# Kernel tuning notes

Hardware: AMD Instinct MI355X
Metric: run time of the kernel (lower is better)

The kernel has to match this reference:

```python
import jax, jax.numpy as jnp
import numpy as np

N_NODES = 50000
N_EDGES = 800000
F_IN = 128
HEADS = 2
C_HID = 64
N_GRAPHS = 32
NEG_SLOPE = 0.2
LP_LAYERS = 2
LP_ALPHA = 0.5


def gatv2_conv(x, src, dst, W_l, W_r, att, bias):
    """GATv2Conv (concat=True), edge_attr=None, self-loops already in src/dst."""
    H, C = att.shape
    N = x.shape[0]
    xl = (x @ W_l).reshape(N, H, C)  # source-side transform (x_j)
    xr = (x @ W_r).reshape(N, H, C)  # target-side transform (x_i)
    xj = xl[src]                      # [E,H,C]
    e = jax.nn.leaky_relu(xr[dst] + xj, NEG_SLOPE)
    logits = jnp.einsum('ehc,hc->eh', e, att)  # [E,H]
    # segment softmax over incoming edges of each target node
    m = jax.ops.segment_max(logits, dst, num_segments=N)
    m = jnp.where(jnp.isfinite(m), m, 0.0)
    p = jnp.exp(logits - m[dst])
    s = jax.ops.segment_sum(p, dst, num_segments=N)
    alpha = p / (s[dst] + 1e-16)
    out = jax.ops.segment_sum(xj * alpha[:, :, None], dst, num_segments=N)
    return out.reshape(N, H * C) + bias


def label_prop(y, src, dst):
    """PyG LabelPropagation: sym gcn_norm (no self-loops), clamp(0,1) post-step."""
    N = y.shape[0]
    ones = jnp.ones(src.shape[0], dtype=y.dtype)
    deg = jax.ops.segment_sum(ones, dst, num_segments=N)
    dinv = jnp.where(deg > 0, jax.lax.rsqrt(jnp.maximum(deg, 1.0)), 0.0)
    w = (dinv[src] * dinv[dst])[:, None]
    res = (1.0 - LP_ALPHA) * y
    out = y
    for _ in range(LP_LAYERS):
        out = LP_ALPHA * jax.ops.segment_sum(out[src] * w, dst, num_segments=N) + res
        out = jnp.clip(out, 0.0, 1.0)
    return out


def setup_inputs() -> dict:
    key = jax.random.key(0)
    ks = jax.random.split(key, 16)
    HC = HEADS * C_HID

    def glorot(k, shape):
        lim = np.sqrt(6.0 / (shape[0] + shape[-1]))
        return jax.random.uniform(k, shape, jnp.float32, -lim, lim)

    x = jax.random.normal(ks[0], (N_NODES, F_IN), jnp.float32)
    edge_index = jax.random.randint(ks[1], (2, N_EDGES), 0, N_NODES, jnp.int32)
    batch = jnp.sort(jax.random.randint(ks[2], (N_NODES,), 0, N_GRAPHS, jnp.int32))
    return {
        'x': x, 'edge_index': edge_index, 'batch': batch,
        'W_l1': glorot(ks[3], (F_IN, HC)), 'W_r1': glorot(ks[4], (F_IN, HC)),
        'att1': glorot(ks[5], (HEADS, C_HID)), 'b1': jnp.zeros((HC,), jnp.float32),
        'W_l2': glorot(ks[6], (HC, HC)), 'W_r2': glorot(ks[7], (HC, HC)),
        'att2': glorot(ks[8], (HEADS, C_HID)), 'b2': jnp.zeros((HC,), jnp.float32),
        'mlp_W1': glorot(ks[9], (F_IN + 2 * HC, 256)), 'mlp_b1': jnp.zeros((256,), jnp.float32),
        'mlp_W2': glorot(ks[10], (256, 128)), 'mlp_b2': jnp.zeros((128,), jnp.float32),
    }


def reference(x, edge_index, batch, W_l1, W_r1, att1, b1, W_l2, W_r2, att2, b2,
              mlp_W1, mlp_b1, mlp_W2, mlp_b2):
    N = x.shape[0]
    src, dst = edge_index[0], edge_index[1]
    # GATv2Conv adds self-loops by default
    loop = jnp.arange(N, dtype=src.dtype)
    src_sl = jnp.concatenate([src, loop])
    dst_sl = jnp.concatenate([dst, loop])

    h0 = x
    h1 = jax.nn.elu(gatv2_conv(h0, src_sl, dst_sl, W_l1, W_r1, att1, b1))
    h1 = label_prop(h1, src, dst)
    h2 = jax.nn.elu(gatv2_conv(h1, src_sl, dst_sl, W_l2, W_r2, att2, b2))
    h2 = label_prop(h2, src, dst)

    combined = jnp.concatenate([h0, h1, h2], axis=-1)  # [N, 384]
    # global mean pool over graphs
    sums = jax.ops.segment_sum(combined, batch, num_segments=N_GRAPHS)
    cnts = jax.ops.segment_sum(jnp.ones((N,), combined.dtype), batch, num_segments=N_GRAPHS)
    g = sums / jnp.maximum(cnts, 1.0)[:, None]  # [G, 384]

    h = jax.nn.relu(g @ mlp_W1 + mlp_b1)  # dropout is identity in eval
    return h @ mlp_W2 + mlp_b2
```

## Files before the change

kernel.cpp:

```cpp
#include <hip/hip_runtime.h>
#include <math.h>

#define FDIM 128
#define NEG_SLOPE 0.2f
#define LP_ALPHA 0.5f
#define NGRAPHS 32
#define POOLF 384
#define MLP_H 256
#define OUT_F 128
#define POOL_CH 8

#define LRELU(z) ((z) > 0.0f ? (z) : NEG_SLOPE * (z))

__global__ void count_deg_k(const int* __restrict__ dst, int* __restrict__ deg, int E) {
    int e = blockIdx.x * blockDim.x + threadIdx.x;
    if (e < E) atomicAdd(&deg[dst[e]], 1);
}

__global__ __launch_bounds__(256) void scan_part_k(const int* __restrict__ deg,
                                                   int* __restrict__ tileSum, int N) {
    int b = blockIdx.x, t = threadIdx.x;
    int base = b * 1024 + t * 4;
    int v = 0;
    if (base + 3 < N) { int4 d = *(const int4*)(deg + base); v = d.x + d.y + d.z + d.w; }
    else if (base < N) {
        v = deg[base];
        if (base + 1 < N) v += deg[base + 1];
        if (base + 2 < N) v += deg[base + 2];
    }
#pragma unroll
    for (int off = 32; off > 0; off >>= 1) v += __shfl_xor(v, off, 64);
    __shared__ int ws[4];
    if ((t & 63) == 0) ws[t >> 6] = v;
    __syncthreads();
    if (t == 0) tileSum[b] = ws[0] + ws[1] + ws[2] + ws[3];
}

__global__ void scan_tiles_k(const int* __restrict__ tileSum, int* __restrict__ tileOff, int nt) {
    int t = threadIdx.x;
    int v = (t < nt) ? tileSum[t] : 0;
    int incl = v;
#pragma unroll
    for (int off = 1; off < 64; off <<= 1) {
        int u = __shfl_up(incl, off, 64);
        if (t >= off) incl += u;
    }
    if (t < nt) tileOff[t] = incl - v;
}

__global__ __launch_bounds__(256) void scan_write_k(const int* __restrict__ deg,
                                                    const int* __restrict__ tileOff,
                                                    int* __restrict__ row_ptr,
                                                    int* __restrict__ cursor,
                                                    float* __restrict__ dinv, int N, int E) {
    int b = blockIdx.x, t = threadIdx.x;
    int base = b * 1024 + t * 4;
    int d0 = 0, d1 = 0, d2 = 0, d3 = 0;
    if (base + 3 < N) { int4 d = *(const int4*)(deg + base); d0 = d.x; d1 = d.y; d2 = d.z; d3 = d.w; }
    else if (base < N) {
        d0 = deg[base];
        if (base + 1 < N) d1 = deg[base + 1];
        if (base + 2 < N) d2 = deg[base + 2];
    }
    int lsum = d0 + d1 + d2 + d3;
    int lane = t & 63, wv = t >> 6;
    int incl = lsum;
#pragma unroll
    for (int off = 1; off < 64; off <<= 1) {
        int u = __shfl_up(incl, off, 64);
        if (lane >= off) incl += u;
    }
    __shared__ int wsum[4];
    if (lane == 63) wsum[wv] = incl;
    __syncthreads();
    int woff = 0;
#pragma unroll
    for (int k = 0; k < 4; ++k) if (k < wv) woff += wsum[k];
    int off0 = tileOff[b] + woff + (incl - lsum);
    if (base < N)     { row_ptr[base]     = off0;                cursor[base]     = off0;
                        dinv[base]     = d0 > 0 ? 1.0f / sqrtf((float)d0) : 0.0f; }
    if (base + 1 < N) { row_ptr[base + 1] = off0 + d0;           cursor[base + 1] = off0 + d0;
                        dinv[base + 1] = d1 > 0 ? 1.0f / sqrtf((float)d1) : 0.0f; }
    if (base + 2 < N) { row_ptr[base + 2] = off0 + d0 + d1;      cursor[base + 2] = off0 + d0 + d1;
                        dinv[base + 2] = d2 > 0 ? 1.0f / sqrtf((float)d2) : 0.0f; }
    if (base + 3 < N) { row_ptr[base + 3] = off0 + d0 + d1 + d2; cursor[base + 3] = off0 + d0 + d1 + d2;
                        dinv[base + 3] = d3 > 0 ? 1.0f / sqrtf((float)d3) : 0.0f; }
    if (b == 0 && t == 0) row_ptr[N] = E;
}

__global__ void scatter_k(const int* __restrict__ src, const int* __restrict__ dst,
                          int* __restrict__ cursor, const float* __restrict__ dinv,
                          int2* __restrict__ elist, int E) {
    int e = blockIdx.x * blockDim.x + threadIdx.x;
    if (e >= E) return;
    int d = dst[e], s = src[e];
    int pos = atomicAdd(&cursor[d], 1);
    unsigned long long v = (unsigned int)s |
                           ((unsigned long long)(unsigned int)__float_as_int(dinv[s]) << 32);
    __builtin_nontemporal_store(v, (unsigned long long*)&elist[pos]);
}

__global__ void gbound_k(const int* __restrict__ batch, int* __restrict__ gb, int N) {
    int g = threadIdx.x;
    if (g > NGRAPHS) return;
    int lo = 0, hi = N;
    while (lo < hi) {
        int mid = (lo + hi) >> 1;
        if (batch[mid] < g) lo = mid + 1; else hi = mid;
    }
    gb[g] = lo;
}

__global__ __launch_bounds__(256) void gemm128x2_k(const float* __restrict__ X,
                                                   const float* __restrict__ Wl,
                                                   const float* __restrict__ Wr,
                                                   float* __restrict__ Yl,
                                                   float* __restrict__ Yr, int N) {
    __shared__ float Xs[FDIM][68];
    int t = threadIdx.x;
    int r0 = blockIdx.x * 64;
    for (int idx = t; idx < 64 * FDIM; idx += 256) {
        int k = idx & 127, r = idx >> 7;
        int row = r0 + r;
        Xs[k][r] = (row < N) ? X[(size_t)row * FDIM + k] : 0.0f;
    }
    __syncthreads();
    int tr = t >> 5;
    int tc = t & 31;
    float accl[8][4] = {{0.f}}, accr[8][4] = {{0.f}};
#pragma unroll 2
    for (int k = 0; k < FDIM; ++k) {
        float4 bl = *(const float4*)(Wl + k * FDIM + tc * 4);
        float4 br = *(const float4*)(Wr + k * FDIM + tc * 4);
        float4 a0 = *(const float4*)(&Xs[k][tr * 8]);
        float4 a1 = *(const float4*)(&Xs[k][tr * 8 + 4]);
        float av[8] = {a0.x, a0.y, a0.z, a0.w, a1.x, a1.y, a1.z, a1.w};
#pragma unroll
        for (int r = 0; r < 8; ++r) {
            accl[r][0] = fmaf(av[r], bl.x, accl[r][0]);
            accl[r][1] = fmaf(av[r], bl.y, accl[r][1]);
            accl[r][2] = fmaf(av[r], bl.z, accl[r][2]);
            accl[r][3] = fmaf(av[r], bl.w, accl[r][3]);
            accr[r][0] = fmaf(av[r], br.x, accr[r][0]);
            accr[r][1] = fmaf(av[r], br.y, accr[r][1]);
            accr[r][2] = fmaf(av[r], br.z, accr[r][2]);
            accr[r][3] = fmaf(av[r], br.w, accr[r][3]);
        }
    }
#pragma unroll
    for (int r = 0; r < 8; ++r) {
        int row = r0 + tr * 8 + r;
        if (row < N) {
            *(float4*)(Yl + (size_t)row * FDIM + tc * 4) =
                make_float4(accl[r][0], accl[r][1], accl[r][2], accl[r][3]);
            *(float4*)(Yr + (size_t)row * FDIM + tc * 4) =
                make_float4(accr[r][0], accr[r][1], accr[r][2], accr[r][3]);
        }
    }
}

__global__ __launch_bounds__(256) void gat_pull_k(const float* __restrict__ xl,
                                                  const float* __restrict__ xr,
                                                  const int* __restrict__ row_ptr,
                                                  const int2* __restrict__ elist,
                                                  const float* __restrict__ att,
                                                  const float* __restrict__ bias,
                                                  float* __restrict__ out, int N) {
    int wid = threadIdx.x >> 6;
    int lane = threadIdx.x & 63;
    int half = lane >> 5;
    int lh = lane & 31;
    int i = blockIdx.x * 4 + wid;
    if (i >= N) return;
    float4 at = *(const float4*)(att + 4 * lh);
    size_t ibase = (size_t)i * FDIM + 4 * lh;
    float4 xrv = *(const float4*)(xr + ibase);
    float4 xs  = *(const float4*)(xl + ibase);

    auto qdot = [&](float4 xv) {
        float v = LRELU(xrv.x + xv.x) * at.x + LRELU(xrv.y + xv.y) * at.y
                + LRELU(xrv.z + xv.z) * at.z + LRELU(xrv.w + xv.w) * at.w;
        v += __shfl_xor(v, 8, 64);
        v += __shfl_xor(v, 4, 64);
        v += __shfl_xor(v, 2, 64);
        v += __shfl_xor(v, 1, 64);
        return v;
    };

    float lself = qdot(xs);
    float m0 = half ? -INFINITY : lself;
    float s0 = half ? 0.0f : 1.0f;
    float4 a0 = half ? make_float4(0.f, 0.f, 0.f, 0.f) : xs;
    float m1 = -INFINITY, s1 = 0.0f;
    float4 a1 = make_float4(0.f, 0.f, 0.f, 0.f);

    int beg = row_ptr[i], end = row_ptr[i + 1];
    for (int p = beg; p < end; p += 4) {
        int i0 = p + half, i1 = p + 2 + half;
        bool v0 = i0 < end, v1 = i1 < end;
        int j0 = elist[min(i0, end - 1)].x;
        int j1 = elist[min(i1, end - 1)].x;
        float4 x0 = *(const float4*)(xl + (size_t)j0 * FDIM + 4 * lh);
        float4 x1 = *(const float4*)(xl + (size_t)j1 * FDIM + 4 * lh);
        float l0 = qdot(x0);
        float l1 = qdot(x1);
        if (v0) {
            float mn = fmaxf(m0, l0);
            float sc = __expf(m0 - mn), pe = __expf(l0 - mn);
            s0 = fmaf(s0, sc, pe);
            a0.x = fmaf(a0.x, sc, pe * x0.x); a0.y = fmaf(a0.y, sc, pe * x0.y);
            a0.z = fmaf(a0.z, sc, pe * x0.z); a0.w = fmaf(a0.w, sc, pe * x0.w);
            m0 = mn;
        }
        if (v1) {
            float mn = fmaxf(m1, l1);
            float sc = __expf(m1 - mn), pe = __expf(l1 - mn);
            s1 = fmaf(s1, sc, pe);
            a1.x = fmaf(a1.x, sc, pe * x1.x); a1.y = fmaf(a1.y, sc, pe * x1.y);
            a1.z = fmaf(a1.z, sc, pe * x1.z); a1.w = fmaf(a1.w, sc, pe * x1.w);
            m1 = mn;
        }
    }
    {
        float mn = fmaxf(m0, m1);
        float c0 = (m0 == -INFINITY) ? 0.0f : __expf(m0 - mn);
        float c1 = (m1 == -INFINITY) ? 0.0f : __expf(m1 - mn);
        s0 = s0 * c0 + s1 * c1;
        a0.x = a0.x * c0 + a1.x * c1; a0.y = a0.y * c0 + a1.y * c1;
        a0.z = a0.z * c0 + a1.z * c1; a0.w = a0.w * c0 + a1.w * c1;
        m0 = mn;
    }
    {
        float pm = __shfl_xor(m0, 32, 64);
        float ps = __shfl_xor(s0, 32, 64);
        float px = __shfl_xor(a0.x, 32, 64), py = __shfl_xor(a0.y, 32, 64);
        float pz = __shfl_xor(a0.z, 32, 64), pw = __shfl_xor(a0.w, 32, 64);
        float mn = fmaxf(m0, pm);
        float c0 = (m0 == -INFINITY) ? 0.0f : __expf(m0 - mn);
        float c1 = (pm == -INFINITY) ? 0.0f : __expf(pm - mn);
        s0 = s0 * c0 + ps * c1;
        a0.x = a0.x * c0 + px * c1; a0.y = a0.y * c0 + py * c1;
        a0.z = a0.z * c0 + pz * c1; a0.w = a0.w * c0 + pw * c1;
    }
    if (half == 0) {
        float inv = 1.0f / (s0 + 1e-16f);
        float4 bv = *(const float4*)(bias + 4 * lh);
        float zx = a0.x * inv + bv.x, zy = a0.y * inv + bv.y;
        float zz = a0.z * inv + bv.z, zw = a0.w * inv + bv.w;
        float4 o;
        o.x = (zx > 0.0f) ? zx : (__expf(zx) - 1.0f);
        o.y = (zy > 0.0f) ? zy : (__expf(zy) - 1.0f);
        o.z = (zz > 0.0f) ? zz : (__expf(zz) - 1.0f);
        o.w = (zw > 0.0f) ? zw : (__expf(zw) - 1.0f);
        *(float4*)(out + ibase) = o;
    }
}

__global__ __launch_bounds__(256) void lp_pull_k(const float* __restrict__ y,
                                                 const float* __restrict__ cur,
                                                 float* __restrict__ nxt,
                                                 const int* __restrict__ row_ptr,
                                                 const int2* __restrict__ elist,
                                                 const float* __restrict__ dinv, int N) {
    int wid = threadIdx.x >> 6, lane = threadIdx.x & 63;
    int half = lane >> 5, lh = lane & 31;
    int i = blockIdx.x * 4 + wid;
    if (i >= N) return;
    int beg = row_ptr[i], end = row_ptr[i + 1];
    float4 a0 = make_float4(0.f, 0.f, 0.f, 0.f), a1 = a0, a2 = a0, a3 = a0;
    for (int p = beg; p < end; p += 8) {
        int i0 = p + half, i1 = p + 2 + half, i2 = p + 4 + half, i3 = p + 6 + half;
        int2 e0 = elist[min(i0, end - 1)];
        int2 e1 = elist[min(i1, end - 1)];
        int2 e2 = elist[min(i2, end - 1)];
        int2 e3 = elist[min(i3, end - 1)];
        float w0 = (i0 < end) ? __int_as_float(e0.y) : 0.0f;
        float w1 = (i1 < end) ? __int_as_float(e1.y) : 0.0f;
        float w2 = (i2 < end) ? __int_as_float(e2.y) : 0.0f;
        float w3 = (i3 < end) ? __int_as_float(e3.y) : 0.0f;
        float4 x0 = *(const float4*)(cur + (size_t)e0.x * FDIM + 4 * lh);
        float4 x1 = *(const float4*)(cur + (size_t)e1.x * FDIM + 4 * lh);
        float4 x2 = *(const float4*)(cur + (size_t)e2.x * FDIM + 4 * lh);
        float4 x3 = *(const float4*)(cur + (size_t)e3.x * FDIM + 4 * lh);
        a0.x = fmaf(w0, x0.x, a0.x); a0.y = fmaf(w0, x0.y, a0.y);
        a0.z = fmaf(w0, x0.z, a0.z); a0.w = fmaf(w0, x0.w, a0.w);
        a1.x = fmaf(w1, x1.x, a1.x); a1.y = fmaf(w1, x1.y, a1.y);
        a1.z = fmaf(w1, x1.z, a1.z); a1.w = fmaf(w1, x1.w, a1.w);
        a2.x = fmaf(w2, x2.x, a2.x); a2.y = fmaf(w2, x2.y, a2.y);
        a2.z = fmaf(w2, x2.z, a2.z); a2.w = fmaf(w2, x2.w, a2.w);
        a3.x = fmaf(w3, x3.x, a3.x); a3.y = fmaf(w3, x3.y, a3.y);
        a3.z = fmaf(w3, x3.z, a3.z); a3.w = fmaf(w3, x3.w, a3.w);
    }
    float4 a;
    a.x = (a0.x + a1.x) + (a2.x + a3.x);
    a.y = (a0.y + a1.y) + (a2.y + a3.y);
    a.z = (a0.z + a1.z) + (a2.z + a3.z);
    a.w = (a0.w + a1.w) + (a2.w + a3.w);
    a.x += __shfl_xor(a.x, 32, 64);
    a.y += __shfl_xor(a.y, 32, 64);
    a.z += __shfl_xor(a.z, 32, 64);
    a.w += __shfl_xor(a.w, 32, 64);
    if (half == 0) {
        float di = dinv[i];
        size_t ibase = (size_t)i * FDIM + 4 * lh;
        float4 yv = *(const float4*)(y + ibase);
        float4 o;
        o.x = fminf(fmaxf(fmaf(LP_ALPHA * di, a.x, (1.0f - LP_ALPHA) * yv.x), 0.f), 1.f);
        o.y = fminf(fmaxf(fmaf(LP_ALPHA * di, a.y, (1.0f - LP_ALPHA) * yv.y), 0.f), 1.f);
        o.z = fminf(fmaxf(fmaf(LP_ALPHA * di, a.z, (1.0f - LP_ALPHA) * yv.z), 0.f), 1.f);
        o.w = fminf(fmaxf(fmaf(LP_ALPHA * di, a.w, (1.0f - LP_ALPHA) * yv.w), 0.f), 1.f);
        *(float4*)(nxt + ibase) = o;
    }
}

__global__ void pool_part_k(const float* __restrict__ x, const float* __restrict__ h1,
                            const float* __restrict__ h2, const int* __restrict__ gb,
                            float* __restrict__ part) {
    int g = blockIdx.x, si = blockIdx.y, ch = blockIdx.z;
    int t = threadIdx.x;
    const float* s = (si == 0) ? x : ((si == 1) ? h1 : h2);
    int n0g = gb[g], n1g = gb[g + 1];
    int len = n1g - n0g;
    int per = (len + POOL_CH - 1) / POOL_CH;
    int n0 = n0g + ch * per;
    int n1 = min(n0 + per, n1g);
    float acc = 0.0f;
    for (int n = n0; n < n1; ++n) acc += s[(size_t)n * FDIM + t];
    part[(((g * 3 + si) << 3) + ch) * FDIM + t] = acc;
}

__global__ void mlp1_k(const float* __restrict__ part, const int* __restrict__ gb,
                       const float* __restrict__ W1, const float* __restrict__ b1,
                       float* __restrict__ h) {
    int g = blockIdx.x;
    int t = threadIdx.x;
    __shared__ float gm[POOLF];
    int cnt = gb[g + 1] - gb[g];
    float inv = 1.0f / fmaxf((float)cnt, 1.0f);
    for (int f = t; f < POOLF; f += 256) {
        int si = f >> 7, fl = f & 127;
        float s = 0.0f;
#pragma unroll
        for (int c = 0; c < POOL_CH; ++c)
            s += part[(((g * 3 + si) << 3) + c) * FDIM + fl];
        gm[f] = s * inv;
    }
    __syncthreads();
    float acc = b1[t];
    for (int k = 0; k < POOLF; ++k) acc = fmaf(gm[k], W1[k * MLP_H + t], acc);
    h[g * MLP_H + t] = fmaxf(acc, 0.0f);
}

__global__ void mlp2_k(const float* __restrict__ h, const float* __restrict__ W2,
                       const float* __restrict__ b2, float* __restrict__ out) {
    int g = blockIdx.x;
    int t = threadIdx.x;
    __shared__ float hs[MLP_H];
    for (int k = t; k < MLP_H; k += 128) hs[k] = h[g * MLP_H + k];
    __syncthreads();
    float acc = b2[t];
    for (int k = 0; k < MLP_H; ++k) acc = fmaf(hs[k], W2[k * OUT_F + t], acc);
    out[g * OUT_F + t] = acc;
}

extern "C" void kernel_launch(void* const* d_in, const int* in_sizes, int n_in,
                              void* d_out, int out_size, void* d_ws, size_t ws_size,
                              hipStream_t stream) {
    const float* x    = (const float*)d_in[0];
    const int*   ei   = (const int*)d_in[1];
    const int*   batch= (const int*)d_in[2];
    const float* W_l1 = (const float*)d_in[3];
    const float* W_r1 = (const float*)d_in[4];
    const float* att1 = (const float*)d_in[5];
    const float* b1   = (const float*)d_in[6];
    const float* W_l2 = (const float*)d_in[7];
    const float* W_r2 = (const float*)d_in[8];
    const float* att2 = (const float*)d_in[9];
    const float* b2   = (const float*)d_in[10];
    const float* mW1  = (const float*)d_in[11];
    const float* mb1  = (const float*)d_in[12];
    const float* mW2  = (const float*)d_in[13];
    const float* mb2  = (const float*)d_in[14];
    float* out = (float*)d_out;

    const int N = in_sizes[2];
    const int E = in_sizes[1] / 2;
    const int* src = ei;
    const int* dst = ei + E;

    char* w = (char*)d_ws;
    auto alloc = [&](size_t bytes) -> char* {
        char* p = w;
        w += (bytes + 255) & ~(size_t)255;
        return p;
    };
    float* bufA = (float*)alloc((size_t)N * FDIM * 4);
    float* bufB = (float*)alloc((size_t)N * FDIM * 4);
    float* bufC = (float*)alloc((size_t)N * FDIM * 4);
    float* bufD = (float*)alloc((size_t)N * FDIM * 4);
    int* deg     = (int*)alloc((size_t)N * 4);
    int* cursor  = (int*)alloc((size_t)N * 4);
    int* row_lp  = (int*)alloc((size_t)(N + 1) * 4);
    int2* elist  = (int2*)alloc((size_t)E * 8);
    float* dinv  = (float*)alloc((size_t)N * 4);
    int* gb      = (int*)alloc((size_t)(NGRAPHS + 1) * 4);
    int* tileSum = (int*)alloc((size_t)64 * 4);
    int* tileOff = (int*)alloc((size_t)64 * 4);
    float* part  = (float*)alloc((size_t)NGRAPHS * 3 * POOL_CH * FDIM * 4);
    float* mlp_h = (float*)alloc((size_t)NGRAPHS * MLP_H * 4);

    const int TB = 256;
    int gE = (E + TB - 1) / TB;
    int nTiles = (N + 1023) / 1024;

    hipMemsetAsync(deg, 0, (size_t)N * 4, stream);
    count_deg_k<<<gE, TB, 0, stream>>>(dst, deg, E);
    gbound_k<<<1, 64, 0, stream>>>(batch, gb, N);
    scan_part_k<<<nTiles, 256, 0, stream>>>(deg, tileSum, N);
    scan_tiles_k<<<1, 64, 0, stream>>>(tileSum, tileOff, nTiles);
    scan_write_k<<<nTiles, 256, 0, stream>>>(deg, tileOff, row_lp, cursor, dinv, N, E);
    scatter_k<<<gE, TB, 0, stream>>>(src, dst, cursor, dinv, elist, E);

    int gGemm = (N + 63) / 64;
    int gWave = (N + 3) / 4;

    gemm128x2_k<<<gGemm, 256, 0, stream>>>(x, W_l1, W_r1, bufA, bufB, N);
    gat_pull_k<<<gWave, 256, 0, stream>>>(bufA, bufB, row_lp, elist, att1, b1, bufC, N);
    lp_pull_k<<<gWave, 256, 0, stream>>>(bufC, bufC, bufA, row_lp, elist, dinv, N);
    lp_pull_k<<<gWave, 256, 0, stream>>>(bufC, bufA, bufC, row_lp, elist, dinv, N);

    gemm128x2_k<<<gGemm, 256, 0, stream>>>(bufC, W_l2, W_r2, bufA, bufB, N);
    gat_pull_k<<<gWave, 256, 0, stream>>>(bufA, bufB, row_lp, elist, att2, b2, bufD, N);
    lp_pull_k<<<gWave, 256, 0, stream>>>(bufD, bufD, bufA, row_lp, elist, dinv, N);
    lp_pull_k<<<gWave, 256, 0, stream>>>(bufD, bufA, bufD, row_lp, elist, dinv, N);

    pool_part_k<<<dim3(NGRAPHS, 3, POOL_CH), 128, 0, stream>>>(x, bufC, bufD, gb, part);

    mlp1_k<<<NGRAPHS, 256, 0, stream>>>(part, gb, mW1, mb1, mlp_h);
    mlp2_k<<<NGRAPHS, 128, 0, stream>>>(mlp_h, mW2, mb2, out);
}
```

Baseline: 739.0 us.

## Process four edges per wave in GAT pull and halve GEMM per-thread rows

The GAT aggregation kernel now splits each wave into four 16-lane groups, each owning 8 channels, so four neighbor edges are gathered concurrently instead of two. This raises memory-level parallelism for the irregular gathers. It costs more registers and an extra cross-group shuffle merge of the online-softmax state. Separately, the dual GEMM kernel now uses 512 threads per 64-row tile with 4 rows per thread, trading register tiling reuse for more threads.

```diff
diff --git a/kernel.cpp b/kernel.cpp
--- a/kernel.cpp
+++ b/kernel.cpp
@@ -111,7 +111,7 @@
     gb[g] = lo;
 }
 
-__global__ __launch_bounds__(256) void gemm128x2_k(const float* __restrict__ X,
+__global__ __launch_bounds__(512) void gemm128x2_k(const float* __restrict__ X,
                                                    const float* __restrict__ Wl,
                                                    const float* __restrict__ Wr,
                                                    float* __restrict__ Yl,
@@ -119,7 +119,7 @@
     __shared__ float Xs[FDIM][68];
     int t = threadIdx.x;
     int r0 = blockIdx.x * 64;
-    for (int idx = t; idx < 64 * FDIM; idx += 256) {
+    for (int idx = t; idx < 64 * FDIM; idx += 512) {
         int k = idx & 127, r = idx >> 7;
         int row = r0 + r;
         Xs[k][r] = (row < N) ? X[(size_t)row * FDIM + k] : 0.0f;
@@ -127,16 +127,15 @@
     __syncthreads();
     int tr = t >> 5;
     int tc = t & 31;
-    float accl[8][4] = {{0.f}}, accr[8][4] = {{0.f}};
-#pragma unroll 2
+    float accl[4][4] = {{0.f}}, accr[4][4] = {{0.f}};
+#pragma unroll 4
     for (int k = 0; k < FDIM; ++k) {
         float4 bl = *(const float4*)(Wl + k * FDIM + tc * 4);
         float4 br = *(const float4*)(Wr + k * FDIM + tc * 4);
-        float4 a0 = *(const float4*)(&Xs[k][tr * 8]);
-        float4 a1 = *(const float4*)(&Xs[k][tr * 8 + 4]);
-        float av[8] = {a0.x, a0.y, a0.z, a0.w, a1.x, a1.y, a1.z, a1.w};
-#pragma unroll
-        for (int r = 0; r < 8; ++r) {
+        float4 a = *(const float4*)(&Xs[k][tr * 4]);
+        float av[4] = {a.x, a.y, a.z, a.w};
+#pragma unroll
+        for (int r = 0; r < 4; ++r) {
             accl[r][0] = fmaf(av[r], bl.x, accl[r][0]);
             accl[r][1] = fmaf(av[r], bl.y, accl[r][1]);
             accl[r][2] = fmaf(av[r], bl.z, accl[r][2]);
@@ -148,8 +147,8 @@
         }
     }
 #pragma unroll
-    for (int r = 0; r < 8; ++r) {
-        int row = r0 + tr * 8 + r;
+    for (int r = 0; r < 4; ++r) {
+        int row = r0 + tr * 4 + r;
         if (row < N) {
             *(float4*)(Yl + (size_t)row * FDIM + tc * 4) =
                 make_float4(accl[r][0], accl[r][1], accl[r][2], accl[r][3]);
@@ -168,91 +167,119 @@
                                                   float* __restrict__ out, int N) {
     int wid = threadIdx.x >> 6;
     int lane = threadIdx.x & 63;
-    int half = lane >> 5;
-    int lh = lane & 31;
+    int qw = lane >> 4;
+    int lq = lane & 15;
     int i = blockIdx.x * 4 + wid;
     if (i >= N) return;
-    float4 at = *(const float4*)(att + 4 * lh);
-    size_t ibase = (size_t)i * FDIM + 4 * lh;
-    float4 xrv = *(const float4*)(xr + ibase);
-    float4 xs  = *(const float4*)(xl + ibase);
-
-    auto qdot = [&](float4 xv) {
-        float v = LRELU(xrv.x + xv.x) * at.x + LRELU(xrv.y + xv.y) * at.y
-                + LRELU(xrv.z + xv.z) * at.z + LRELU(xrv.w + xv.w) * at.w;
-        v += __shfl_xor(v, 8, 64);
+    int cbase = 8 * lq;
+    float4 at0 = *(const float4*)(att + cbase);
+    float4 at1 = *(const float4*)(att + cbase + 4);
+    size_t ibase = (size_t)i * FDIM + cbase;
+    float4 xr0 = *(const float4*)(xr + ibase);
+    float4 xr1 = *(const float4*)(xr + ibase + 4);
+    float4 xs0 = *(const float4*)(xl + ibase);
+    float4 xs1 = *(const float4*)(xl + ibase + 4);
+
+    auto qdot = [&](float4 x0, float4 x1) {
+        float v = LRELU(xr0.x + x0.x) * at0.x + LRELU(xr0.y + x0.y) * at0.y
+                + LRELU(xr0.z + x0.z) * at0.z + LRELU(xr0.w + x0.w) * at0.w
+                + LRELU(xr1.x + x1.x) * at1.x + LRELU(xr1.y + x1.y) * at1.y
+                + LRELU(xr1.z + x1.z) * at1.z + LRELU(xr1.w + x1.w) * at1.w;
+        v += __shfl_xor(v, 1, 64);
+        v += __shfl_xor(v, 2, 64);
         v += __shfl_xor(v, 4, 64);
-        v += __shfl_xor(v, 2, 64);
-        v += __shfl_xor(v, 1, 64);
         return v;
     };
 
-    float lself = qdot(xs);
-    float m0 = half ? -INFINITY : lself;
-    float s0 = half ? 0.0f : 1.0f;
-    float4 a0 = half ? make_float4(0.f, 0.f, 0.f, 0.f) : xs;
-    float m1 = -INFINITY, s1 = 0.0f;
-    float4 a1 = make_float4(0.f, 0.f, 0.f, 0.f);
+    const float4 z4 = make_float4(0.f, 0.f, 0.f, 0.f);
+    float lself = qdot(xs0, xs1);
+    bool q0 = (qw == 0);
+    float mA = q0 ? lself : -INFINITY, sA = q0 ? 1.0f : 0.0f;
+    float4 aA0 = q0 ? xs0 : z4, aA1 = q0 ? xs1 : z4;
+    float mB = -INFINITY, sB = 0.0f;
+    float4 aB0 = z4, aB1 = z4;
 
     int beg = row_ptr[i], end = row_ptr[i + 1];
-    for (int p = beg; p < end; p += 4) {
-        int i0 = p + half, i1 = p + 2 + half;
+    for (int p = beg; p < end; p += 8) {
+        int i0 = p + qw, i1 = p + 4 + qw;
         bool v0 = i0 < end, v1 = i1 < end;
         int j0 = elist[min(i0, end - 1)].x;
         int j1 = elist[min(i1, end - 1)].x;
-        float4 x0 = *(const float4*)(xl + (size_t)j0 * FDIM + 4 * lh);
-        float4 x1 = *(const float4*)(xl + (size_t)j1 * FDIM + 4 * lh);
-        float l0 = qdot(x0);
-        float l1 = qdot(x1);
+        const float* b0 = xl + (size_t)j0 * FDIM + cbase;
+        const float* b1 = xl + (size_t)j1 * FDIM + cbase;
+        float4 x00 = *(const float4*)(b0), x01 = *(const float4*)(b0 + 4);
+        float4 x10 = *(const float4*)(b1), x11 = *(const float4*)(b1 + 4);
+        float l0 = qdot(x00, x01);
+        float l1 = qdot(x10, x11);
         if (v0) {
-            float mn = fmaxf(m0, l0);
-            float sc = __expf(m0 - mn), pe = __expf(l0 - mn);
-            s0 = fmaf(s0, sc, pe);
-            a0.x = fmaf(a0.x, sc, pe * x0.x); a0.y = fmaf(a0.y, sc, pe * x0.y);
-            a0.z = fmaf(a0.z, sc, pe * x0.z); a0.w = fmaf(a0.w, sc, pe * x0.w);
-            m0 = mn;
+            float mn = fmaxf(mA, l0);
+            float sc = __expf(mA - mn), pe = __expf(l0 - mn);
+            sA = fmaf(sA, sc, pe);
+            aA0.x = fmaf(aA0.x, sc, pe * x00.x); aA0.y = fmaf(aA0.y, sc, pe * x00.y);
+            aA0.z = fmaf(aA0.z, sc, pe * x00.z); aA0.w = fmaf(aA0.w, sc, pe * x00.w);
+            aA1.x = fmaf(aA1.x, sc, pe * x01.x); aA1.y = fmaf(aA1.y, sc, pe * x01.y);
+            aA1.z = fmaf(aA1.z, sc, pe * x01.z); aA1.w = fmaf(aA1.w, sc, pe * x01.w);
+            mA = mn;
         }
         if (v1) {
-            float mn = fmaxf(m1, l1);
-            float sc = __expf(m1 - mn), pe = __expf(l1 - mn);
-            s1 = fmaf(s1, sc, pe);
-            a1.x = fmaf(a1.x, sc, pe * x1.x); a1.y = fmaf(a1.y, sc, pe * x1.y);
-            a1.z = fmaf(a1.z, sc, pe * x1.z); a1.w = fmaf(a1.w, sc, pe * x1.w);
-            m1 = mn;
+            float mn = fmaxf(mB, l1);
+            float sc = __expf(mB - mn), pe = __expf(l1 - mn);
+            sB = fmaf(sB, sc, pe);
+            aB0.x = fmaf(aB0.x, sc, pe * x10.x); aB0.y = fmaf(aB0.y, sc, pe * x10.y);
+            aB0.z = fmaf(aB0.z, sc, pe * x10.z); aB0.w = fmaf(aB0.w, sc, pe * x10.w);
+            aB1.x = fmaf(aB1.x, sc, pe * x11.x); aB1.y = fmaf(aB1.y, sc, pe * x11.y);
+            aB1.z = fmaf(aB1.z, sc, pe * x11.z); aB1.w = fmaf(aB1.w, sc, pe * x11.w);
+            mB = mn;
         }
     }
     {
-        float mn = fmaxf(m0, m1);
-        float c0 = (m0 == -INFINITY) ? 0.0f : __expf(m0 - mn);
-        float c1 = (m1 == -INFINITY) ? 0.0f : __expf(m1 - mn);
-        s0 = s0 * c0 + s1 * c1;
-        a0.x = a0.x * c0 + a1.x * c1; a0.y = a0.y * c0 + a1.y * c1;
-        a0.z = a0.z * c0 + a1.z * c1; a0.w = a0.w * c0 + a1.w * c1;
-        m0 = mn;
-    }
-    {
-        float pm = __shfl_xor(m0, 32, 64);
-        float ps = __shfl_xor(s0, 32, 64);
-        float px = __shfl_xor(a0.x, 32, 64), py = __shfl_xor(a0.y, 32, 64);
-        float pz = __shfl_xor(a0.z, 32, 64), pw = __shfl_xor(a0.w, 32, 64);
-        float mn = fmaxf(m0, pm);
-        float c0 = (m0 == -INFINITY) ? 0.0f : __expf(m0 - mn);
-        float c1 = (pm == -INFINITY) ? 0.0f : __expf(pm - mn);
-        s0 = s0 * c0 + ps * c1;
-        a0.x = a0.x * c0 + px * c1; a0.y = a0.y * c0 + py * c1;
-        a0.z = a0.z * c0 + pz * c1; a0.w = a0.w * c0 + pw * c1;
-    }
-    if (half == 0) {
-        float inv = 1.0f / (s0 + 1e-16f);
-        float4 bv = *(const float4*)(bias + 4 * lh);
-        float zx = a0.x * inv + bv.x, zy = a0.y * inv + bv.y;
-        float zz = a0.z * inv + bv.z, zw = a0.w * inv + bv.w;
-        float4 o;
-        o.x = (zx > 0.0f) ? zx : (__expf(zx) - 1.0f);
-        o.y = (zy > 0.0f) ? zy : (__expf(zy) - 1.0f);
-        o.z = (zz > 0.0f) ? zz : (__expf(zz) - 1.0f);
-        o.w = (zw > 0.0f) ? zw : (__expf(zw) - 1.0f);
-        *(float4*)(out + ibase) = o;
+        float mn = fmaxf(mA, mB);
+        float cA = (mA == -INFINITY) ? 0.0f : __expf(mA - mn);
+        float cB = (mB == -INFINITY) ? 0.0f : __expf(mB - mn);
+        sA = sA * cA + sB * cB;
+        aA0.x = aA0.x * cA + aB0.x * cB; aA0.y = aA0.y * cA + aB0.y * cB;
+        aA0.z = aA0.z * cA + aB0.z * cB; aA0.w = aA0.w * cA + aB0.w * cB;
+        aA1.x = aA1.x * cA + aB1.x * cB; aA1.y = aA1.y * cA + aB1.y * cB;
+        aA1.z = aA1.z * cA + aB1.z * cB; aA1.w = aA1.w * cA + aB1.w * cB;
+        mA = mn;
+    }
+#pragma unroll
+    for (int mask = 16; mask <= 32; mask <<= 1) {
+        float pm = __shfl_xor(mA, mask, 64);
+        float ps = __shfl_xor(sA, mask, 64);
+        float p0x = __shfl_xor(aA0.x, mask, 64), p0y = __shfl_xor(aA0.y, mask, 64);
+        float p0z = __shfl_xor(aA0.z, mask, 64), p0w = __shfl_xor(aA0.w, mask, 64);
+        float p1x = __shfl_xor(aA1.x, mask, 64), p1y = __shfl_xor(aA1.y, mask, 64);
+        float p1z = __shfl_xor(aA1.z, mask, 64), p1w = __shfl_xor(aA1.w, mask, 64);
+        float mn = fmaxf(mA, pm);
+        float cA = (mA == -INFINITY) ? 0.0f : __expf(mA - mn);
+        float cP = (pm == -INFINITY) ? 0.0f : __expf(pm - mn);
+        sA = sA * cA + ps * cP;
+        aA0.x = aA0.x * cA + p0x * cP; aA0.y = aA0.y * cA + p0y * cP;
+        aA0.z = aA0.z * cA + p0z * cP; aA0.w = aA0.w * cA + p0w * cP;
+        aA1.x = aA1.x * cA + p1x * cP; aA1.y = aA1.y * cA + p1y * cP;
+        aA1.z = aA1.z * cA + p1z * cP; aA1.w = aA1.w * cA + p1w * cP;
+        mA = mn;
+    }
+    if (qw == 0) {
+        float inv = 1.0f / (sA + 1e-16f);
+        float4 bv0 = *(const float4*)(bias + cbase);
+        float4 bv1 = *(const float4*)(bias + cbase + 4);
+        float z0 = aA0.x * inv + bv0.x, z1 = aA0.y * inv + bv0.y;
+        float z2 = aA0.z * inv + bv0.z, z3 = aA0.w * inv + bv0.w;
+        float z4_ = aA1.x * inv + bv1.x, z5 = aA1.y * inv + bv1.y;
+        float z6 = aA1.z * inv + bv1.z, z7 = aA1.w * inv + bv1.w;
+        float4 o0, o1;
+        o0.x = (z0 > 0.f) ? z0 : (__expf(z0) - 1.f);
+        o0.y = (z1 > 0.f) ? z1 : (__expf(z1) - 1.f);
+        o0.z = (z2 > 0.f) ? z2 : (__expf(z2) - 1.f);
+        o0.w = (z3 > 0.f) ? z3 : (__expf(z3) - 1.f);
+        o1.x = (z4_ > 0.f) ? z4_ : (__expf(z4_) - 1.f);
+        o1.y = (z5 > 0.f) ? z5 : (__expf(z5) - 1.f);
+        o1.z = (z6 > 0.f) ? z6 : (__expf(z6) - 1.f);
+        o1.w = (z7 > 0.f) ? z7 : (__expf(z7) - 1.f);
+        *(float4*)(out + ibase) = o0;
+        *(float4*)(out + ibase + 4) = o1;
     }
 }
 
@@ -424,12 +451,12 @@
     int gGemm = (N + 63) / 64;
     int gWave = (N + 3) / 4;
 
-    gemm128x2_k<<<gGemm, 256, 0, stream>>>(x, W_l1, W_r1, bufA, bufB, N);
+    gemm128x2_k<<<gGemm, 512, 0, stream>>>(x, W_l1, W_r1, bufA, bufB, N);
     gat_pull_k<<<gWave, 256, 0, stream>>>(bufA, bufB, row_lp, elist, att1, b1, bufC, N);
     lp_pull_k<<<gWave, 256, 0, stream>>>(bufC, bufC, bufA, row_lp, elist, dinv, N);
     lp_pull_k<<<gWave, 256, 0, stream>>>(bufC, bufA, bufC, row_lp, elist, dinv, N);
 
-    gemm128x2_k<<<gGemm, 256, 0, stream>>>(bufC, W_l2, W_r2, bufA, bufB, N);
+    gemm128x2_k<<<gGemm, 512, 0, stream>>>(bufC, W_l2, W_r2, bufA, bufB, N);
     gat_pull_k<<<gWave, 256, 0, stream>>>(bufA, bufB, row_lp, elist, att2, b2, bufD, N);
     lp_pull_k<<<gWave, 256, 0, stream>>>(bufD, bufD, bufA, row_lp, elist, dinv, N);
     lp_pull_k<<<gWave, 256, 0, stream>>>(bufD, bufA, bufD, row_lp, elist, dinv, N);
```

Result: slower. 781.5 us (+5.8%).
